# Performance work log

Measured on AMD Instinct MI355X. Metric: run time of the kernel, lower is better.

The kernel has to match this reference:

```python
import jax, jax.numpy as jnp
import numpy as np

N = 50000
IN_DIM, HID_DIM, OUT_DIM = 512, 256, 64
E = 800000


def setup_inputs() -> dict:
    key = jax.random.key(0)
    k1, k2, k3, k4, k5, k6 = jax.random.split(key, 6)
    x = jax.random.normal(k1, (N, IN_DIM), dtype=jnp.float32)
    edge_index = jax.random.randint(k2, (2, E), 0, N, dtype=jnp.int64)
    # GCNConv parameters (glorot-ish scale)
    W1 = jax.random.normal(k3, (IN_DIM, HID_DIM), dtype=jnp.float32) * (1.0 / np.sqrt(IN_DIM))
    b1 = jnp.zeros((HID_DIM,), dtype=jnp.float32)
    W2 = jax.random.normal(k4, (HID_DIM, OUT_DIM), dtype=jnp.float32) * (1.0 / np.sqrt(HID_DIM))
    b2 = jnp.zeros((OUT_DIM,), dtype=jnp.float32)
    return {"x": x, "W1": W1, "b1": b1, "W2": W2, "b2": b2, "edge_index": edge_index}


def _gcn_conv(x, W, b, src, dst, norm, n_nodes):
    # PyG GCNConv: out[dst] = sum_e norm_e * (x @ W)[src_e] + b
    h = x @ W                              # [N, out]
    msg = h[src] * norm[:, None]           # [E+N, out] gather + scale
    out = jax.ops.segment_sum(msg, dst, num_segments=n_nodes)  # scatter-add
    return out + b


def reference(x, W1, b1, W2, b2, edge_index):
    n = x.shape[0]
    # add self-loops (PyG default add_self_loops=True)
    loop = jnp.arange(n, dtype=edge_index.dtype)
    src = jnp.concatenate([edge_index[0], loop])
    dst = jnp.concatenate([edge_index[1], loop])
    # symmetric normalization: deg computed on destination (in-degree incl. self-loop)
    deg = jax.ops.segment_sum(jnp.ones_like(dst, dtype=x.dtype), dst, num_segments=n)
    dis = jnp.where(deg > 0, jax.lax.rsqrt(jnp.maximum(deg, 1.0)), 0.0)
    norm = dis[src] * dis[dst]
    h = _gcn_conv(x, W1, b1, src, dst, norm, n)
    h = jax.nn.relu(h)
    out = _gcn_conv(h, W2, b2, src, dst, norm, n)
    return out
```

## Files before the change

### kernel.cpp

```cpp
#include <hip/hip_runtime.h>
#include <hip/hip_bf16.h>
#include <hip/hip_fp16.h>
#include <stdint.h>

typedef _Float16 half8_t __attribute__((ext_vector_type(8)));
typedef float f32x4_t __attribute__((ext_vector_type(4)));


__global__ __launch_bounds__(256) void detect_i64_kernel(const int* __restrict__ idx,
                                                         int* __restrict__ flag,
                                                         int* __restrict__ bcnt) {
    int t = threadIdx.x;
    if (t < 64) {
        int v = idx[2 * t + 1];
        unsigned long long b = __ballot(v == 0);
        if (t == 0) *flag = (b == 0xFFFFFFFFFFFFFFFFULL) ? 1 : 0;
    }
    bcnt[t] = 0;
}

__device__ __forceinline__ int load_idx(const int* __restrict__ idx, long long pos, int is64) {
    return is64 ? idx[2 * pos] : idx[pos];
}

#define EPB 4096

__global__ __launch_bounds__(256) void bin_count_kernel(
        const int* __restrict__ idx, const int* __restrict__ flag,
        int* __restrict__ bcnt, int E, int N) {
    __shared__ int hist[256];
    hist[threadIdx.x] = 0;
    __syncthreads();
    const int is64 = *flag;
    const int base = blockIdx.x * EPB;
    const int cnt = (E - base < EPB) ? E - base : EPB;
    for (int i = threadIdx.x; i < cnt; i += 256) {
        int d = load_idx(idx, (long long)E + base + i, is64);
        if ((unsigned)d < (unsigned)N) atomicAdd(&hist[d >> 8], 1);
    }
    __syncthreads();
    int h = hist[threadIdx.x];
    if (h) atomicAdd(&bcnt[threadIdx.x], h);
}

__global__ __launch_bounds__(256) void scan_buckets_kernel(
        const int* __restrict__ bcnt, int* __restrict__ bbase,
        int* __restrict__ bcur, int NB) {
    __shared__ int buf[256];
    int t = threadIdx.x;
    int v = (t < NB) ? bcnt[t] : 0;
    buf[t] = v;
    __syncthreads();
    #pragma unroll
    for (int off = 1; off < 256; off <<= 1) {
        int u = (t >= off) ? buf[t - off] : 0;
        __syncthreads();
        buf[t] += u;
        __syncthreads();
    }
    int excl = buf[t] - v;
    if (t < NB) { bbase[t] = excl; bcur[t] = excl; }
    if (t == NB - 1) bbase[NB] = buf[t];
}

__global__ __launch_bounds__(256) void bin_scatter_kernel(
        const int* __restrict__ idx, const int* __restrict__ flag,
        int* __restrict__ bcur, unsigned* __restrict__ packed, int E, int N) {
    __shared__ int cur[256];
    cur[threadIdx.x] = 0;
    __syncthreads();
    const int is64 = *flag;
    const int base = blockIdx.x * EPB;
    const int cnt = (E - base < EPB) ? E - base : EPB;
    for (int i = threadIdx.x; i < cnt; i += 256) {
        int d = load_idx(idx, (long long)E + base + i, is64);
        if ((unsigned)d < (unsigned)N) atomicAdd(&cur[d >> 8], 1);
    }
    __syncthreads();
    int h = cur[threadIdx.x];
    int bs = h ? atomicAdd(&bcur[threadIdx.x], h) : 0;
    __syncthreads();
    cur[threadIdx.x] = bs;
    __syncthreads();
    for (int i = threadIdx.x; i < cnt; i += 256) {
        int d = load_idx(idx, (long long)E + base + i, is64);
        if ((unsigned)d >= (unsigned)N) continue;
        int s = load_idx(idx, base + i, is64);
        if ((unsigned)s >= (unsigned)N) s = 0;
        int pos = atomicAdd(&cur[d >> 8], 1);
        packed[pos] = (unsigned)s | ((unsigned)(d & 255) << 16);
    }
}

__global__ __launch_bounds__(256) void bucket_sort_kernel(
        const unsigned* __restrict__ packed, const int* __restrict__ bbase,
        int* __restrict__ csr_src, int* __restrict__ offsets,
        float* __restrict__ dis, int N, int NB) {
    __shared__ int buf[256];
    __shared__ int cur[256];
    const int b = blockIdx.x;
    const int t = threadIdx.x;
    cur[t] = 0;
    __syncthreads();
    const int e0 = bbase[b], e1 = bbase[b + 1];
    for (int i = e0 + t; i < e1; i += 256)
        atomicAdd(&cur[(packed[i] >> 16) & 255], 1);
    __syncthreads();
    int v = cur[t];
    buf[t] = v;
    __syncthreads();
    #pragma unroll
    for (int off = 1; off < 256; off <<= 1) {
        int u = (t >= off) ? buf[t - off] : 0;
        __syncthreads();
        buf[t] += u;
        __syncthreads();
    }
    int excl = buf[t] - v;
    cur[t] = excl;
    int node = b * 256 + t;
    if (node < N) {
        offsets[node] = e0 + excl;
        dis[node] = rsqrtf((float)(v + 1));
    }
    if (b == NB - 1 && t == 0) offsets[N] = bbase[NB];
    __syncthreads();
    for (int i = e0 + t; i < e1; i += 256) {
        unsigned rec = packed[i];
        int dl = (rec >> 16) & 255;
        int pos = atomicAdd(&cur[dl], 1);
        csr_src[e0 + pos] = (int)(rec & 0xFFFF);
    }
}

__global__ void wt_kernel(const float* __restrict__ W1, const float* __restrict__ W2,
                          _Float16* __restrict__ w1t, _Float16* __restrict__ w2t) {
    int p = blockIdx.x * 256 + threadIdx.x;
    if (p < 512 * 256) {
        int k = p >> 8, n = p & 255;
        w1t[n * 512 + k] = (_Float16)W1[p];
    } else {
        int q = p - 512 * 256;
        if (q < 256 * 64) {
            int k = q >> 6, n = q & 63;
            w2t[n * 256 + k] = (_Float16)W2[q];
        }
    }
}

__global__ __launch_bounds__(256, 3) void gemm1_kernel(
        const float* __restrict__ x, const _Float16* __restrict__ w1t,
        const float* __restrict__ dis, _Float16* __restrict__ h1s, int M) {
    __shared__ _Float16 As[8 * 65 * 8];
    __shared__ _Float16 Bs[8 * 257 * 8];
    const int tid = threadIdx.x;
    const int brow = blockIdx.x * 64;
    const int w = tid >> 6, lane = tid & 63;
    const int wcol = w * 64;
    const int lrow = lane & 15, lkb = lane >> 4;

    const int arow = tid >> 2, akq = tid & 3;
    const int gr = brow + arow;
    const bool aval = gr < M;
    const float* xptr = x + (size_t)(aval ? gr : 0) * 512 + akq * 16;
    const _Float16* bptr = w1t + (size_t)tid * 512;
    const int awr0 = ((akq * 2) * 65 + arow) << 3;
    const int awr1 = ((akq * 2 + 1) * 65 + arow) << 3;

    f32x4_t acc[4][4];
    #pragma unroll
    for (int mi = 0; mi < 4; ++mi)
        #pragma unroll
        for (int nj = 0; nj < 4; ++nj) acc[mi][nj] = (f32x4_t)0.f;

    float4 a0 = make_float4(0,0,0,0), a1 = a0, a2 = a0, a3 = a0;
    half8_t b[8];

    if (aval) {
        a0 = *(const float4*)(xptr);
        a1 = *(const float4*)(xptr + 4);
        a2 = *(const float4*)(xptr + 8);
        a3 = *(const float4*)(xptr + 12);
    }
    #pragma unroll
    for (int kb = 0; kb < 8; ++kb) b[kb] = *(const half8_t*)(bptr + kb * 8);

    for (int t = 0; t < 8; ++t) {
        __syncthreads();
        half8_t h0, h1;
        h0[0] = (_Float16)a0.x; h0[1] = (_Float16)a0.y;
        h0[2] = (_Float16)a0.z; h0[3] = (_Float16)a0.w;
        h0[4] = (_Float16)a1.x; h0[5] = (_Float16)a1.y;
        h0[6] = (_Float16)a1.z; h0[7] = (_Float16)a1.w;
        h1[0] = (_Float16)a2.x; h1[1] = (_Float16)a2.y;
        h1[2] = (_Float16)a2.z; h1[3] = (_Float16)a2.w;
        h1[4] = (_Float16)a3.x; h1[5] = (_Float16)a3.y;
        h1[6] = (_Float16)a3.z; h1[7] = (_Float16)a3.w;
        *(half8_t*)&As[awr0] = h0;
        *(half8_t*)&As[awr1] = h1;
        #pragma unroll
        for (int kb = 0; kb < 8; ++kb)
            *(half8_t*)&Bs[(kb * 257 + tid) << 3] = b[kb];
        __syncthreads();
        if (t < 7) {
            int k0 = (t + 1) * 64;
            if (aval) {
                a0 = *(const float4*)(xptr + k0);
                a1 = *(const float4*)(xptr + k0 + 4);
                a2 = *(const float4*)(xptr + k0 + 8);
                a3 = *(const float4*)(xptr + k0 + 12);
            }
            #pragma unroll
            for (int kb = 0; kb < 8; ++kb)
                b[kb] = *(const half8_t*)(bptr + k0 + kb * 8);
        }
        #pragma unroll
        for (int h = 0; h < 2; ++h) {
            half8_t af[4], bf[4];
            #pragma unroll
            for (int mi = 0; mi < 4; ++mi)
                af[mi] = *(const half8_t*)&As[((h * 4 + lkb) * 65 + mi * 16 + lrow) << 3];
            #pragma unroll
            for (int nj = 0; nj < 4; ++nj)
                bf[nj] = *(const half8_t*)&Bs[((h * 4 + lkb) * 257 + wcol + nj * 16 + lrow) << 3];
            #pragma unroll
            for (int mi = 0; mi < 4; ++mi)
                #pragma unroll
                for (int nj = 0; nj < 4; ++nj)
                    acc[mi][nj] = __builtin_amdgcn_mfma_f32_16x16x32_f16(af[mi], bf[nj], acc[mi][nj], 0, 0, 0);
        }
    }
    #pragma unroll
    for (int mi = 0; mi < 4; ++mi) {
        #pragma unroll
        for (int r = 0; r < 4; ++r) {
            int grow = brow + mi * 16 + (lane >> 4) * 4 + r;
            if (grow >= M) continue;
            float s = dis[grow];
            #pragma unroll
            for (int nj = 0; nj < 4; ++nj) {
                int col = wcol + nj * 16 + lrow;
                h1s[((size_t)(col >> 5) * M + grow) * 32 + (col & 31)] =
                    (_Float16)(acc[mi][nj][r] * s);
            }
        }
    }
}

__global__ __launch_bounds__(256, 4) void gemm2_kernel(
        const _Float16* __restrict__ a1s, const _Float16* __restrict__ w2t,
        const float* __restrict__ dis, _Float16* __restrict__ h2s, int M) {
    __shared__ _Float16 As[4 * 65 * 8];
    __shared__ _Float16 Bs[4 * 65 * 8];
    const int tid = threadIdx.x;
    const int brow = blockIdx.x * 64;
    const int w = tid >> 6, lane = tid & 63;
    const int lrow = lane & 15, lkb = lane >> 4;

    const int arow = tid >> 2, akb = tid & 3;
    const int gr = brow + arow;
    const bool aval = gr < M;
    const _Float16* aptr = a1s + ((size_t)(aval ? gr : 0)) * 32 + akb * 8;
    const _Float16* bptr = w2t + (size_t)arow * 256 + akb * 8;
    const int awr = (akb * 65 + arow) << 3;

    f32x4_t acc[4];
    #pragma unroll
    for (int nj = 0; nj < 4; ++nj) acc[nj] = (f32x4_t)0.f;

    const half8_t zero8 = (half8_t)(_Float16)0.f;
    half8_t ah = zero8, bh;
    if (aval) ah = *(const half8_t*)(aptr);
    bh = *(const half8_t*)(bptr);

    for (int t = 0; t < 8; ++t) {
        __syncthreads();
        *(half8_t*)&As[awr] = ah;
        *(half8_t*)&Bs[awr] = bh;
        __syncthreads();
        if (t < 7) {
            if (aval) ah = *(const half8_t*)(aptr + (size_t)(t + 1) * M * 32);
            bh = *(const half8_t*)(bptr + (t + 1) * 32);
        }
        half8_t a = *(const half8_t*)&As[(lkb * 65 + w * 16 + lrow) << 3];
        half8_t b[4];
        #pragma unroll
        for (int nj = 0; nj < 4; ++nj)
            b[nj] = *(const half8_t*)&Bs[(lkb * 65 + nj * 16 + lrow) << 3];
        #pragma unroll
        for (int nj = 0; nj < 4; ++nj)
            acc[nj] = __builtin_amdgcn_mfma_f32_16x16x32_f16(a, b[nj], acc[nj], 0, 0, 0);
    }
    #pragma unroll
    for (int r = 0; r < 4; ++r) {
        int grow = brow + w * 16 + (lane >> 4) * 4 + r;
        if (grow >= M) continue;
        float s = dis[grow];
        #pragma unroll
        for (int nj = 0; nj < 4; ++nj) {
            int col = nj * 16 + lrow;
            h2s[((size_t)(col >> 5) * M + grow) * 32 + (col & 31)] =
                (_Float16)(acc[nj][r] * s);
        }
    }
}

__device__ __forceinline__ float4 up4(uint2 v) {
    __half2 h0 = *reinterpret_cast<__half2*>(&v.x);
    __half2 h1 = *reinterpret_cast<__half2*>(&v.y);
    float2 a = __half22float2(h0), b = __half22float2(h1);
    return make_float4(a.x, a.y, b.x, b.y);
}

__device__ __forceinline__ unsigned pkw(unsigned a, unsigned b) {
    __half2 ha = *reinterpret_cast<__half2*>(&a);
    __half2 hb = *reinterpret_cast<__half2*>(&b);
    __half2 r = __hadd2(ha, hb);
    return *reinterpret_cast<unsigned*>(&r);
}

__device__ __forceinline__ uint4 pk4(uint4 a, uint4 b) {
    uint4 r;
    r.x = pkw(a.x, b.x);
    r.y = pkw(a.y, b.y);
    r.z = pkw(a.z, b.z);
    r.w = pkw(a.w, b.w);
    return r;
}

template<int NCH, int FP16OUT>
__global__ __launch_bounds__(256) void aggv_kernel(
        const _Float16* __restrict__ g, const int* __restrict__ offsets,
        const int* __restrict__ csr_src, const float* __restrict__ dis,
        const float* __restrict__ bias, void* __restrict__ out, int N) {
    constexpr int CAP = 2048;
    __shared__ int lds_csr[CAP];
    const int chunk = blockIdx.x % NCH;
    const int nodeBase = (blockIdx.x / NCH) * 64;
    const int grp = threadIdx.x >> 2;
    const int cl = threadIdx.x & 3;
    const int node = nodeBase + grp;
    const bool active = node < N;
    const int nend = (nodeBase + 64 < N) ? nodeBase + 64 : N;
    const int blk0 = offsets[nodeBase];
    const int blk1 = offsets[nend];
    const uint4* gc = (const uint4*)g + (size_t)chunk * N * 4;

    int gs0 = 0, gs1 = 0;
    float s = 0.f;
    if (active) { gs0 = offsets[node]; gs1 = offsets[node + 1]; s = dis[node]; }

    float4 accLo = make_float4(0.f, 0.f, 0.f, 0.f);
    float4 accHi = make_float4(0.f, 0.f, 0.f, 0.f);
    if (active) {
        uint4 sv = gc[(size_t)node * 4 + cl];
        float4 lo = up4(make_uint2(sv.x, sv.y));
        float4 hi = up4(make_uint2(sv.z, sv.w));
        accLo.x += lo.x; accLo.y += lo.y; accLo.z += lo.z; accLo.w += lo.w;
        accHi.x += hi.x; accHi.y += hi.y; accHi.z += hi.z; accHi.w += hi.w;
    }

    for (int base = blk0; base < blk1; base += CAP) {
        const int cnt = (blk1 - base < CAP) ? blk1 - base : CAP;
        __syncthreads();
        for (int i = threadIdx.x; i < cnt; i += 256)
            lds_csr[i] = csr_src[base + i];
        __syncthreads();
        int lo_e = (gs0 > base ? gs0 : base) - base;
        int hi_e = (gs1 < base + cnt ? gs1 : base + cnt) - base;
        int e = lo_e;
        for (; e + 4 <= hi_e; e += 4) {
            int s0 = lds_csr[e], s1 = lds_csr[e + 1];
            int s2 = lds_csr[e + 2], s3 = lds_csr[e + 3];
            uint4 v0 = gc[(size_t)s0 * 4 + cl];
            uint4 v1 = gc[(size_t)s1 * 4 + cl];
            uint4 v2 = gc[(size_t)s2 * 4 + cl];
            uint4 v3 = gc[(size_t)s3 * 4 + cl];
            uint4 q = pk4(pk4(v0, v1), pk4(v2, v3));
            float4 flo = up4(make_uint2(q.x, q.y));
            float4 fhi = up4(make_uint2(q.z, q.w));
            accLo.x += flo.x; accLo.y += flo.y; accLo.z += flo.z; accLo.w += flo.w;
            accHi.x += fhi.x; accHi.y += fhi.y; accHi.z += fhi.z; accHi.w += fhi.w;
        }
        for (; e < hi_e; ++e) {
            int s0 = lds_csr[e];
            uint4 v = gc[(size_t)s0 * 4 + cl];
            float4 flo = up4(make_uint2(v.x, v.y));
            float4 fhi = up4(make_uint2(v.z, v.w));
            accLo.x += flo.x; accLo.y += flo.y; accLo.z += flo.z; accLo.w += flo.w;
            accHi.x += fhi.x; accHi.y += fhi.y; accHi.z += fhi.z; accHi.w += fhi.w;
        }
    }
    if (active) {
        float4 bb0 = *(const float4*)&bias[chunk * 32 + cl * 8];
        float4 bb1 = *(const float4*)&bias[chunk * 32 + cl * 8 + 4];
        float4 o0, o1;
        o0.x = fmaf(s, accLo.x, bb0.x);
        o0.y = fmaf(s, accLo.y, bb0.y);
        o0.z = fmaf(s, accLo.z, bb0.z);
        o0.w = fmaf(s, accLo.w, bb0.w);
        o1.x = fmaf(s, accHi.x, bb1.x);
        o1.y = fmaf(s, accHi.y, bb1.y);
        o1.z = fmaf(s, accHi.z, bb1.z);
        o1.w = fmaf(s, accHi.w, bb1.w);
        if (FP16OUT) {
            o0.x = fmaxf(o0.x, 0.f); o0.y = fmaxf(o0.y, 0.f);
            o0.z = fmaxf(o0.z, 0.f); o0.w = fmaxf(o0.w, 0.f);
            o1.x = fmaxf(o1.x, 0.f); o1.y = fmaxf(o1.y, 0.f);
            o1.z = fmaxf(o1.z, 0.f); o1.w = fmaxf(o1.w, 0.f);
            __half2 p0 = __float22half2_rn(make_float2(o0.x, o0.y));
            __half2 p1 = __float22half2_rn(make_float2(o0.z, o0.w));
            __half2 p2 = __float22half2_rn(make_float2(o1.x, o1.y));
            __half2 p3 = __float22half2_rn(make_float2(o1.z, o1.w));
            uint4 pv;
            pv.x = *reinterpret_cast<unsigned*>(&p0);
            pv.y = *reinterpret_cast<unsigned*>(&p1);
            pv.z = *reinterpret_cast<unsigned*>(&p2);
            pv.w = *reinterpret_cast<unsigned*>(&p3);
            ((uint4*)out)[((size_t)chunk * N + node) * 4 + cl] = pv;
        } else {
            ((float4*)out)[(size_t)node * (NCH * 8) + chunk * 8 + cl * 2]     = o0;
            ((float4*)out)[(size_t)node * (NCH * 8) + chunk * 8 + cl * 2 + 1] = o1;
        }
    }
}

extern "C" void kernel_launch(void* const* d_in, const int* in_sizes, int n_in,
                              void* d_out, int out_size, void* d_ws, size_t ws_size,
                              hipStream_t stream) {
    const float* x  = (const float*)d_in[0];
    const float* W1 = (const float*)d_in[1];
    const float* b1 = (const float*)d_in[2];
    const float* W2 = (const float*)d_in[3];
    const float* b2 = (const float*)d_in[4];
    const int* eidx = (const int*)d_in[5];

    const int HID = in_sizes[2];
    const int OUT = in_sizes[4];
    const int IN  = in_sizes[1] / HID;
    const int N   = in_sizes[0] / IN;
    const int E   = in_sizes[5] / 2;
    const int NB  = (N + 255) >> 8;

    char* ws = (char*)d_ws;
    size_t off = 0;
    auto alloc = [&](size_t bytes) {
        off = (off + 255) & ~(size_t)255;
        char* p = ws + off;
        off += bytes;
        return p;
    };
    float* dis       = (float*)alloc((size_t)N * 4);
    int* flag        = (int*)alloc(256);
    int* bcnt        = (int*)alloc(256 * 4);
    int* bbase       = (int*)alloc(260 * 4);
    int* bcur        = (int*)alloc(256 * 4);
    int* offsets     = (int*)alloc((size_t)(N + 1) * 4);
    unsigned* packed = (unsigned*)alloc((size_t)E * 4);
    int* csr_src     = (int*)alloc((size_t)E * 4);
    _Float16* w1t    = (_Float16*)alloc((size_t)IN * HID * 2);
    _Float16* w2t    = (_Float16*)alloc((size_t)HID * OUT * 2);
    _Float16* h1s    = (_Float16*)alloc((size_t)N * HID * 2);
    _Float16* a1s    = (_Float16*)alloc((size_t)N * HID * 2);
    _Float16* h2s    = (_Float16*)alloc((size_t)N * OUT * 2);

    const int nblkE = (E + EPB - 1) / EPB;

    detect_i64_kernel<<<1, 256, 0, stream>>>(eidx, flag, bcnt);
    bin_count_kernel<<<nblkE, 256, 0, stream>>>(eidx, flag, bcnt, E, N);
    scan_buckets_kernel<<<1, 256, 0, stream>>>(bcnt, bbase, bcur, NB);
    bin_scatter_kernel<<<nblkE, 256, 0, stream>>>(eidx, flag, bcur, packed, E, N);
    bucket_sort_kernel<<<NB, 256, 0, stream>>>(packed, bbase, csr_src, offsets, dis, N, NB);
    wt_kernel<<<(IN * HID + HID * OUT + 255) / 256, 256, 0, stream>>>(W1, W2, w1t, w2t);

    gemm1_kernel<<<(N + 63) / 64, 256, 0, stream>>>(x, w1t, dis, h1s, N);
    aggv_kernel<8, 1><<<((N + 63) / 64) * 8, 256, 0, stream>>>(h1s, offsets, csr_src, dis,
                                                               b1, a1s, N);
    gemm2_kernel<<<(N + 63) / 64, 256, 0, stream>>>(a1s, w2t, dis, h2s, N);
    aggv_kernel<2, 0><<<((N + 63) / 64) * 2, 256, 0, stream>>>(h2s, offsets, csr_src, dis,
                                                               b2, d_out, N);
}
```

Before: 170.4 us.

## Shrink gemm1 tile to 32 rows and 32-wide K steps for more blocks

Restructures the first GEMM to process 32-row tiles with a 32-element K step instead of 64x64. This halves the accumulator registers and shared memory per block, raises launch bounds to 4 blocks per SM, and doubles the grid to spread the x-read-bound work across more CUs. The cost is twice as many W1 tile loads per row and twice as many K-loop iterations with barriers.

```diff
diff --git a/kernel.cpp b/kernel.cpp
--- a/kernel.cpp
+++ b/kernel.cpp
@@ -4,6 +4,7 @@
 #include <stdint.h>
 
 typedef _Float16 half8_t __attribute__((ext_vector_type(8)));
+typedef _Float16 half4_t __attribute__((ext_vector_type(4)));
 typedef float f32x4_t __attribute__((ext_vector_type(4)));
 
 
@@ -148,90 +149,74 @@
     }
 }
 
-__global__ __launch_bounds__(256, 3) void gemm1_kernel(
+__global__ __launch_bounds__(256, 4) void gemm1_kernel(
         const float* __restrict__ x, const _Float16* __restrict__ w1t,
         const float* __restrict__ dis, _Float16* __restrict__ h1s, int M) {
-    __shared__ _Float16 As[8 * 65 * 8];
-    __shared__ _Float16 Bs[8 * 257 * 8];
+    __shared__ _Float16 As[4 * 33 * 8];
+    __shared__ _Float16 Bs[4 * 257 * 8];
     const int tid = threadIdx.x;
-    const int brow = blockIdx.x * 64;
+    const int brow = blockIdx.x * 32;
     const int w = tid >> 6, lane = tid & 63;
     const int wcol = w * 64;
     const int lrow = lane & 15, lkb = lane >> 4;
 
-    const int arow = tid >> 2, akq = tid & 3;
+    const int arow = tid >> 3, akb = (tid >> 1) & 3, ahalf = tid & 1;
     const int gr = brow + arow;
     const bool aval = gr < M;
-    const float* xptr = x + (size_t)(aval ? gr : 0) * 512 + akq * 16;
-    const _Float16* bptr = w1t + (size_t)tid * 512;
-    const int awr0 = ((akq * 2) * 65 + arow) << 3;
-    const int awr1 = ((akq * 2 + 1) * 65 + arow) << 3;
-
-    f32x4_t acc[4][4];
-    #pragma unroll
-    for (int mi = 0; mi < 4; ++mi)
+    const float* xptr = x + (size_t)(aval ? gr : 0) * 512 + akb * 8 + ahalf * 4;
+    const _Float16* bbase = w1t + (size_t)(tid >> 2) * 512 + (tid & 3) * 8;
+    const int awr = ((akb * 33 + arow) << 3) + ahalf * 4;
+    const int bwr0 = (((tid & 3) * 257 + (tid >> 2)) << 3);
+
+    f32x4_t acc[2][4];
+    #pragma unroll
+    for (int mi = 0; mi < 2; ++mi)
         #pragma unroll
         for (int nj = 0; nj < 4; ++nj) acc[mi][nj] = (f32x4_t)0.f;
 
-    float4 a0 = make_float4(0,0,0,0), a1 = a0, a2 = a0, a3 = a0;
-    half8_t b[8];
-
-    if (aval) {
-        a0 = *(const float4*)(xptr);
-        a1 = *(const float4*)(xptr + 4);
-        a2 = *(const float4*)(xptr + 8);
-        a3 = *(const float4*)(xptr + 12);
-    }
-    #pragma unroll
-    for (int kb = 0; kb < 8; ++kb) b[kb] = *(const half8_t*)(bptr + kb * 8);
-
-    for (int t = 0; t < 8; ++t) {
-        __syncthreads();
-        half8_t h0, h1;
-        h0[0] = (_Float16)a0.x; h0[1] = (_Float16)a0.y;
-        h0[2] = (_Float16)a0.z; h0[3] = (_Float16)a0.w;
-        h0[4] = (_Float16)a1.x; h0[5] = (_Float16)a1.y;
-        h0[6] = (_Float16)a1.z; h0[7] = (_Float16)a1.w;
-        h1[0] = (_Float16)a2.x; h1[1] = (_Float16)a2.y;
-        h1[2] = (_Float16)a2.z; h1[3] = (_Float16)a2.w;
-        h1[4] = (_Float16)a3.x; h1[5] = (_Float16)a3.y;
-        h1[6] = (_Float16)a3.z; h1[7] = (_Float16)a3.w;
-        *(half8_t*)&As[awr0] = h0;
-        *(half8_t*)&As[awr1] = h1;
-        #pragma unroll
-        for (int kb = 0; kb < 8; ++kb)
-            *(half8_t*)&Bs[(kb * 257 + tid) << 3] = b[kb];
-        __syncthreads();
-        if (t < 7) {
-            int k0 = (t + 1) * 64;
-            if (aval) {
-                a0 = *(const float4*)(xptr + k0);
-                a1 = *(const float4*)(xptr + k0 + 4);
-                a2 = *(const float4*)(xptr + k0 + 8);
-                a3 = *(const float4*)(xptr + k0 + 12);
-            }
-            #pragma unroll
-            for (int kb = 0; kb < 8; ++kb)
-                b[kb] = *(const half8_t*)(bptr + k0 + kb * 8);
-        }
-        #pragma unroll
-        for (int h = 0; h < 2; ++h) {
-            half8_t af[4], bf[4];
-            #pragma unroll
-            for (int mi = 0; mi < 4; ++mi)
-                af[mi] = *(const half8_t*)&As[((h * 4 + lkb) * 65 + mi * 16 + lrow) << 3];
+    float4 av = make_float4(0.f, 0.f, 0.f, 0.f);
+    half8_t bh0, bh1, bh2, bh3;
+
+    if (aval) av = *(const float4*)(xptr);
+    bh0 = *(const half8_t*)(bbase);
+    bh1 = *(const half8_t*)(bbase + 64 * 512);
+    bh2 = *(const half8_t*)(bbase + 128 * 512);
+    bh3 = *(const half8_t*)(bbase + 192 * 512);
+
+    for (int t = 0; t < 16; ++t) {
+        __syncthreads();
+        half4_t ha;
+        ha[0] = (_Float16)av.x; ha[1] = (_Float16)av.y;
+        ha[2] = (_Float16)av.z; ha[3] = (_Float16)av.w;
+        *(half4_t*)&As[awr] = ha;
+        *(half8_t*)&Bs[bwr0] = bh0;
+        *(half8_t*)&Bs[bwr0 + 64 * 8] = bh1;
+        *(half8_t*)&Bs[bwr0 + 128 * 8] = bh2;
+        *(half8_t*)&Bs[bwr0 + 192 * 8] = bh3;
+        __syncthreads();
+        if (t < 15) {
+            int k0 = (t + 1) * 32;
+            if (aval) av = *(const float4*)(xptr + k0);
+            bh0 = *(const half8_t*)(bbase + k0);
+            bh1 = *(const half8_t*)(bbase + k0 + 64 * 512);
+            bh2 = *(const half8_t*)(bbase + k0 + 128 * 512);
+            bh3 = *(const half8_t*)(bbase + k0 + 192 * 512);
+        }
+        half8_t af[2], bf[4];
+        #pragma unroll
+        for (int mi = 0; mi < 2; ++mi)
+            af[mi] = *(const half8_t*)&As[(lkb * 33 + mi * 16 + lrow) << 3];
+        #pragma unroll
+        for (int nj = 0; nj < 4; ++nj)
+            bf[nj] = *(const half8_t*)&Bs[(lkb * 257 + wcol + nj * 16 + lrow) << 3];
+        #pragma unroll
+        for (int mi = 0; mi < 2; ++mi)
             #pragma unroll
             for (int nj = 0; nj < 4; ++nj)
-                bf[nj] = *(const half8_t*)&Bs[((h * 4 + lkb) * 257 + wcol + nj * 16 + lrow) << 3];
-            #pragma unroll
-            for (int mi = 0; mi < 4; ++mi)
-                #pragma unroll
-                for (int nj = 0; nj < 4; ++nj)
-                    acc[mi][nj] = __builtin_amdgcn_mfma_f32_16x16x32_f16(af[mi], bf[nj], acc[mi][nj], 0, 0, 0);
-        }
-    }
-    #pragma unroll
-    for (int mi = 0; mi < 4; ++mi) {
+                acc[mi][nj] = __builtin_amdgcn_mfma_f32_16x16x32_f16(af[mi], bf[nj], acc[mi][nj], 0, 0, 0);
+    }
+    #pragma unroll
+    for (int mi = 0; mi < 2; ++mi) {
         #pragma unroll
         for (int r = 0; r < 4; ++r) {
             int grow = brow + mi * 16 + (lane >> 4) * 4 + r;
@@ -473,7 +458,7 @@
     bucket_sort_kernel<<<NB, 256, 0, stream>>>(packed, bbase, csr_src, offsets, dis, N, NB);
     wt_kernel<<<(IN * HID + HID * OUT + 255) / 256, 256, 0, stream>>>(W1, W2, w1t, w2t);
 
-    gemm1_kernel<<<(N + 63) / 64, 256, 0, stream>>>(x, w1t, dis, h1s, N);
+    gemm1_kernel<<<(N + 31) / 32, 256, 0, stream>>>(x, w1t, dis, h1s, N);
     aggv_kernel<8, 1><<<((N + 63) / 64) * 8, 256, 0, stream>>>(h1s, offsets, csr_src, dis,
                                                                b1, a1s, N);
     gemm2_kernel<<<(N + 63) / 64, 256, 0, stream>>>(a1s, w2t, dis, h2s, N);
```

Result: faster. 158.1 us (-7.2%).
